# Kernel tuning notes

Measured on AMD Instinct MI355X. Metric: run time of the kernel, lower is better.

## Reference

```python
import jax, jax.numpy as jnp
import numpy as np

NZ, NX, NY = 128, 256, 256
N_GAUSS = 50000
SIGMA_CUTOFF = 3.0
R = 3  # hardcoded stencil radius in voxelize()


def setup_inputs() -> dict:
    key = jax.random.key(0)
    k1, k2, k3, k4 = jax.random.split(key, 4)
    centers = jax.random.uniform(k1, (N_GAUSS, 3), jnp.float32) * 2.0 - 1.0
    log_scales = jnp.full((N_GAUSS, 3), -4.0, jnp.float32)
    rho_real = jax.random.normal(k2, (N_GAUSS,), jnp.float32) * 0.1
    rho_imag = jax.random.normal(k3, (N_GAUSS,), jnp.float32) * 0.1
    # k-space undersampling mask (0/1)
    mask = (jax.random.uniform(k4, (NZ, NX, NY), jnp.float32) < 0.3).astype(jnp.float32)
    return {"mask": mask, "centers": centers, "log_scales": log_scales,
            "rho_real": rho_real, "rho_imag": rho_imag}


def _voxelize(centers, log_scales, rho_real, rho_imag):
    gr = jnp.arange(-R, R + 1)
    kz, kx, ky = jnp.meshgrid(gr, gr, gr, indexing='ij')
    offsets = jnp.stack([kz, kx, ky], axis=-1).reshape(-1, 3)  # [K,3], K=343
    dims = jnp.array([NZ, NX, NY], jnp.int32)
    gsm1 = (dims - 1).astype(jnp.float32)  # grid_size - 1
    # nearest voxel of each gaussian center ([-1,1] -> grid coords)
    ci = jnp.round((centers + 1.0) * 0.5 * gsm1).astype(jnp.int32)  # [M,3]
    ni = ci[:, None, :] + offsets[None, :, :]                        # [M,K,3]
    in_bounds = jnp.all((ni >= 0) & (ni < dims), axis=-1)            # [M,K]
    # neighbor coords back in normalized [-1,1] space
    nc = ni.astype(jnp.float32) / gsm1 * 2.0 - 1.0                   # [M,K,3]
    scales = jnp.exp(log_scales)
    delta = (nc - centers[:, None, :]) / (scales[:, None, :] + 1e-8)
    dist_sq = jnp.sum(delta * delta, axis=-1)                        # [M,K]
    valid = in_bounds & (dist_sq <= SIGMA_CUTOFF ** 2)
    w = jnp.where(valid, jnp.exp(-0.5 * dist_sq), 0.0)               # [M,K]
    vals_r = (rho_real[:, None] * w).ravel()
    vals_i = (rho_imag[:, None] * w).ravel()
    # clip indices for safety; invalid entries contribute 0
    nic = jnp.clip(ni, 0, dims - 1)
    flat = ((nic[..., 0] * NX + nic[..., 1]) * NY + nic[..., 2]).ravel()
    vol_r = jnp.zeros(NZ * NX * NY, jnp.float32).at[flat].add(vals_r).reshape(NZ, NX, NY)
    vol_i = jnp.zeros(NZ * NX * NY, jnp.float32).at[flat].add(vals_i).reshape(NZ, NX, NY)
    return vol_r + 1j * vol_i


def _image_to_kspace(vol):
    # centered orthonormal 3D FFT (standard MRI convention)
    return jnp.fft.fftshift(jnp.fft.fftn(jnp.fft.ifftshift(vol), norm='ortho'))


def reference(mask, centers, log_scales, rho_real, rho_imag):
    volume = _voxelize(centers, log_scales, rho_real, rho_imag)
    kspace_pred = mask * _image_to_kspace(volume)
    return (volume, kspace_pred)
```

## Files before the change

### kernel.cpp

```cpp
#include <hip/hip_runtime.h>
#include <math.h>

#define NZd 128
#define NXd 256
#define NYd 256
#define NVOX (NZd * NXd * NYd)
#define PI_F 3.14159265358979323846f
#define SCALE_ORTHO 3.4526698300124393e-4f
#define CAP 512

__global__ void zero_kernel(float4* __restrict__ p, int n4) {
    int i = blockIdx.x * blockDim.x + threadIdx.x;
    if (i < n4) p[i] = make_float4(0.f, 0.f, 0.f, 0.f);
}
__global__ void zero_ints_kernel(int* __restrict__ p, int n) {
    int i = blockIdx.x * blockDim.x + threadIdx.x;
    if (i < n) p[i] = 0;
}

__global__ void voxelize_kernel(const float* __restrict__ centers,
                                const float* __restrict__ log_scales,
                                const float* __restrict__ rho_r,
                                const float* __restrict__ rho_i,
                                float* __restrict__ vol, int M) {
    long long t = (long long)blockIdx.x * blockDim.x + threadIdx.x;
    if (t >= (long long)M * 343) return;
    int g = (int)(t / 343);
    int k = (int)(t % 343);
    int oz = k / 49 - 3, ox = (k / 7) % 7 - 3, oy = k % 7 - 3;
    float cz = centers[g * 3 + 0], cx = centers[g * 3 + 1], cy = centers[g * 3 + 2];
    int iz = (int)rintf((cz + 1.0f) * 0.5f * 127.0f);
    int ix = (int)rintf((cx + 1.0f) * 0.5f * 255.0f);
    int iy = (int)rintf((cy + 1.0f) * 0.5f * 255.0f);
    int nz = iz + oz, nx = ix + ox, ny = iy + oy;
    if (nz < 0 || nz >= NZd || nx < 0 || nx >= NXd || ny < 0 || ny >= NYd) return;
    float sz = expf(log_scales[g * 3 + 0]) + 1e-8f;
    float sx = expf(log_scales[g * 3 + 1]) + 1e-8f;
    float sy = expf(log_scales[g * 3 + 2]) + 1e-8f;
    float dz = ((float)nz / 127.0f * 2.0f - 1.0f - cz) / sz;
    float dx = ((float)nx / 255.0f * 2.0f - 1.0f - cx) / sx;
    float dy = ((float)ny / 255.0f * 2.0f - 1.0f - cy) / sy;
    float d2 = dz * dz + dx * dx + dy * dy;
    if (d2 > 9.0f) return;
    float w = expf(-0.5f * d2);
    int idx = (nz * NXd + nx) * NYd + ny;
    atomicAdd(&vol[2 * idx + 0], rho_r[g] * w);
    atomicAdd(&vol[2 * idx + 1], rho_i[g] * w);
}

__global__ void copy_real_kernel(const float2* __restrict__ cvol,
                                 float* __restrict__ out) {
    int i = blockIdx.x * blockDim.x + threadIdx.x;
    out[i] = cvol[i].x;
}

__device__ __forceinline__ void center_voxel(const float* __restrict__ centers,
                                             int g, int& iz, int& ix, int& iy) {
    float cz = centers[g * 3 + 0], cx = centers[g * 3 + 1], cy = centers[g * 3 + 2];
    iz = min(max((int)rintf((cz + 1.0f) * 0.5f * 127.0f), 0), 127);
    ix = min(max((int)rintf((cx + 1.0f) * 0.5f * 255.0f), 0), 255);
    iy = min(max((int)rintf((cy + 1.0f) * 0.5f * 255.0f), 0), 255);
}

__global__ void bin_count_kernel(const float* __restrict__ centers,
                                 int* __restrict__ cnt, int M) {
    int g = blockIdx.x * blockDim.x + threadIdx.x;
    if (g >= M) return;
    int iz, ix, iy;
    center_voxel(centers, g, iz, ix, iy);
    atomicAdd(&cnt[((iz >> 4) << 8) | ((ix >> 4) << 4) | (iy >> 4)], 1);
}

__global__ void bin_scan_kernel(const int* __restrict__ cnt,
                                int* __restrict__ off,
                                int* __restrict__ cursor) {
    int lane = threadIdx.x;
    int base = lane << 5;
    int s = 0;
    #pragma unroll
    for (int i = 0; i < 32; i++) s += cnt[base + i];
    int incl = s;
    #pragma unroll
    for (int d = 1; d < 64; d <<= 1) {
        int v = __shfl_up(incl, d, 64);
        if (lane >= d) incl += v;
    }
    int run = incl - s;
    for (int i = 0; i < 32; i++) {
        int c = cnt[base + i];
        off[base + i] = run;
        cursor[base + i] = run;
        run += c;
    }
}

__global__ void bin_scatter_kernel(const float* __restrict__ centers,
                                   const float* __restrict__ log_scales,
                                   const float* __restrict__ rho_r,
                                   const float* __restrict__ rho_i,
                                   int* __restrict__ cursor,
                                   int* __restrict__ ciA,
                                   float* __restrict__ czA, float* __restrict__ cxA,
                                   float* __restrict__ cyA,
                                   float* __restrict__ iszA, float* __restrict__ isxA,
                                   float* __restrict__ isyA,
                                   float* __restrict__ rrA, float* __restrict__ riA,
                                   int M) {
    int g = blockIdx.x * blockDim.x + threadIdx.x;
    if (g >= M) return;
    int iz, ix, iy;
    center_voxel(centers, g, iz, ix, iy);
    int b = ((iz >> 4) << 8) | ((ix >> 4) << 4) | (iy >> 4);
    int pos = atomicAdd(&cursor[b], 1);
    ciA[pos] = (iz << 16) | (ix << 8) | iy;
    czA[pos] = centers[g * 3 + 0];
    cxA[pos] = centers[g * 3 + 1];
    cyA[pos] = centers[g * 3 + 2];
    iszA[pos] = 1.0f / (expf(log_scales[g * 3 + 0]) + 1e-8f);
    isxA[pos] = 1.0f / (expf(log_scales[g * 3 + 1]) + 1e-8f);
    isyA[pos] = 1.0f / (expf(log_scales[g * 3 + 2]) + 1e-8f);
    rrA[pos] = rho_r[g];
    riA[pos] = rho_i[g];
}

__global__ __launch_bounds__(256) void tile_accum_kernel(
        const int* __restrict__ cnt, const int* __restrict__ off,
        const int* __restrict__ ciA,
        const float* __restrict__ czA, const float* __restrict__ cxA,
        const float* __restrict__ cyA,
        const float* __restrict__ iszA, const float* __restrict__ isxA,
        const float* __restrict__ isyA,
        const float* __restrict__ rrA, const float* __restrict__ riA,
        float2* __restrict__ cvol, float* __restrict__ out_vr) {
    __shared__ int   sci[CAP];
    __shared__ float scz[CAP], scx[CAP], scy[CAP];
    __shared__ float sisz[CAP], sisx[CAP], sisy[CAP];
    __shared__ float srr[CAP], sri[CAP];
    __shared__ int wcnt[4];

    int tile = blockIdx.x;
    int ty = tile & 15, tx = (tile >> 4) & 15, tz = tile >> 8;
    int z0 = tz << 3, x0 = tx << 4, y0 = ty << 4;
    int t = threadIdx.x;
    int lane = t & 63, wid = t >> 6;
    int yl = t & 15, xl = t >> 4;
    int nx = x0 + xl, ny = y0 + yl;
    float nxf = (float)nx * (2.0f / 255.0f) - 1.0f;
    float nyf = (float)ny * (2.0f / 255.0f) - 1.0f;

    float accR[8], accI[8], zfs[8];
    #pragma unroll
    for (int i = 0; i < 8; i++) {
        accR[i] = 0.f; accI[i] = 0.f;
        zfs[i] = (float)(z0 + i) * (2.0f / 127.0f) - 1.0f;
    }

    int lc = 0;
    int bzl = max(z0 - 3, 0) >> 4,  bzh = min(z0 + 10, 127) >> 4;
    int bxl = max(x0 - 3, 0) >> 4,  bxh = min(x0 + 18, 255) >> 4;
    int byl = max(y0 - 3, 0) >> 4,  byh = min(y0 + 18, 255) >> 4;

    for (int bz = bzl; bz <= bzh; bz++) {
        for (int bx = bxl; bx <= bxh; bx++) {
            int bl = (bz << 8) | (bx << 4) | byl;
            int bh = (bz << 8) | (bx << 4) | byh;
            int qs = off[bl];
            int qe = off[bh] + cnt[bh];
            for (int q0 = qs; q0 < qe; q0 += 256) {
                int q = q0 + t;
                bool keep = false;
                int cpv = 0;
                float czv, cxv, cyv, iszv, isxv, isyv, rrv, riv;
                if (q < qe) {
                    cpv = ciA[q];
                    int iz = cpv >> 16, ix = (cpv >> 8) & 255, iy = cpv & 255;
                    keep = !(ix + 3 < x0 || ix > x0 + 18 ||
                             iy + 3 < y0 || iy > y0 + 18 ||
                             iz + 3 < z0 || iz > z0 + 10);
                }
                if (keep) {
                    czv = czA[q]; cxv = cxA[q]; cyv = cyA[q];
                    iszv = iszA[q]; isxv = isxA[q]; isyv = isyA[q];
                    rrv = rrA[q]; riv = riA[q];
                }
                unsigned long long m = __ballot(keep);
                __syncthreads();
                if (lane == 0) wcnt[wid] = __popcll(m);
                __syncthreads();
                int ntot = wcnt[0] + wcnt[1] + wcnt[2] + wcnt[3];
                if (lc + ntot > CAP) {
                    for (int u = 0; u < lc; u++) {
                        int cp = sci[u];
                        int iz = cp >> 16, ix = (cp >> 8) & 255, iy = cp & 255;
                        int dxi = nx - ix, dyi = ny - iy;
                        if (dxi < -3 || dxi > 3 || dyi < -3 || dyi > 3) continue;
                        float dxv = (nxf - scx[u]) * sisx[u];
                        float dyv = (nyf - scy[u]) * sisy[u];
                        float dxy2 = dxv * dxv + dyv * dyv;
                        if (dxy2 > 9.0f) continue;
                        float cz_ = scz[u], isz_ = sisz[u];
                        float rr = srr[u], ri = sri[u];
                        int zlo = max(z0, iz - 3) - z0;
                        int zhi = min(z0 + 7, iz + 3) - z0;
                        #pragma unroll
                        for (int zl = 0; zl < 8; zl++) {
                            if (zl >= zlo && zl <= zhi) {
                                float dzv = (zfs[zl] - cz_) * isz_;
                                float d2 = dxy2 + dzv * dzv;
                                if (d2 <= 9.0f) {
                                    float w = __expf(-0.5f * d2);
                                    accR[zl] += rr * w;
                                    accI[zl] += ri * w;
                                }
                            }
                        }
                    }
                    __syncthreads();
                    lc = 0;
                }
                int basew = lc;
                #pragma unroll
                for (int w = 0; w < 4; w++) if (w < wid) basew += wcnt[w];
                if (keep) {
                    int pos = basew + __popcll(m & ((1ULL << lane) - 1));
                    sci[pos] = cpv;
                    scz[pos] = czv; scx[pos] = cxv; scy[pos] = cyv;
                    sisz[pos] = iszv; sisx[pos] = isxv; sisy[pos] = isyv;
                    srr[pos] = rrv; sri[pos] = riv;
                }
                lc += ntot;
            }
        }
    }
    __syncthreads();
    for (int u = 0; u < lc; u++) {
        int cp = sci[u];
        int iz = cp >> 16, ix = (cp >> 8) & 255, iy = cp & 255;
        int dxi = nx - ix, dyi = ny - iy;
        if (dxi < -3 || dxi > 3 || dyi < -3 || dyi > 3) continue;
        float dxv = (nxf - scx[u]) * sisx[u];
        float dyv = (nyf - scy[u]) * sisy[u];
        float dxy2 = dxv * dxv + dyv * dyv;
        if (dxy2 > 9.0f) continue;
        float cz_ = scz[u], isz_ = sisz[u];
        float rr = srr[u], ri = sri[u];
        int zlo = max(z0, iz - 3) - z0;
        int zhi = min(z0 + 7, iz + 3) - z0;
        #pragma unroll
        for (int zl = 0; zl < 8; zl++) {
            if (zl >= zlo && zl <= zhi) {
                float dzv = (zfs[zl] - cz_) * isz_;
                float d2 = dxy2 + dzv * dzv;
                if (d2 <= 9.0f) {
                    float w = __expf(-0.5f * d2);
                    accR[zl] += rr * w;
                    accI[zl] += ri * w;
                }
            }
        }
    }

    #pragma unroll
    for (int zl = 0; zl < 8; zl++) {
        size_t idx = ((size_t)(z0 + zl) * NXd + nx) * NYd + ny;
        cvol[idx] = make_float2(accR[zl], accI[zl]);
        out_vr[idx] = accR[zl];
    }
}

template <int L>
__device__ __forceinline__ void fft_lds(float2* buf) {
    int tid = threadIdx.x;
    for (int half = 1; half < L; half <<= 1) {
        __syncthreads();
        int j = tid & (half - 1);
        int i0 = ((tid ^ j) << 1) | j;
        int i1 = i0 + half;
        float ang = -PI_F * (float)j / (float)half;
        float s, c;
        sincosf(ang, &s, &c);
        float2 a = buf[i0];
        float2 b = buf[i1];
        float tr = c * b.x - s * b.y;
        float ti = c * b.y + s * b.x;
        buf[i0] = make_float2(a.x + tr, a.y + ti);
        buf[i1] = make_float2(a.x - tr, a.y - ti);
    }
    __syncthreads();
}

__global__ void fft_y_kernel(const float2* __restrict__ src,
                             float2* __restrict__ dst) {
    __shared__ float2 buf[256];
    __shared__ float2 tw[128];
    int l = blockIdx.x;
    int tid = threadIdx.x;
    {
        float s, c;
        sincosf(-PI_F * (float)tid / 128.0f, &s, &c);
        tw[tid] = make_float2(c, s);
    }
    int p = ((l >> 8) + l) & 1;
    const float2* s = src + (size_t)l * NYd;
    for (int i = tid; i < 256; i += 128) {
        float2 v = s[i];
        if ((p + i) & 1) { v.x = -v.x; v.y = -v.y; }
        buf[__brev((unsigned)i) >> 24] = v;
    }
    #pragma unroll
    for (int st = 0; st < 8; st++) {
        const int half = 1 << st;
        const int twstep = 128 >> st;
        __syncthreads();
        int j = tid & (half - 1);
        int i0 = ((tid ^ j) << 1) | j;
        int i1 = i0 + half;
        float2 w = tw[j * twstep];
        float2 a = buf[i0];
        float2 b = buf[i1];
        float tr = w.x * b.x - w.y * b.y;
        float ti = w.x * b.y + w.y * b.x;
        buf[i0] = make_float2(a.x + tr, a.y + ti);
        buf[i1] = make_float2(a.x - tr, a.y - ti);
    }
    __syncthreads();
    float2* d = dst + (size_t)l * NYd;
    for (int i = tid; i < 256; i += 128) d[i] = buf[i];
}

__global__ void fft_x_kernel(float2* __restrict__ ks) {
    __shared__ float2 buf[256];
    int l = blockIdx.x;
    int tid = threadIdx.x;
    int z = l >> 8, y = l & 255;
    float2* base = ks + (size_t)z * (NXd * NYd) + y;
    for (int i = tid; i < 256; i += 128)
        buf[__brev((unsigned)i) >> 24] = base[(size_t)i * NYd];
    fft_lds<256>(buf);
    for (int i = tid; i < 256; i += 128)
        base[(size_t)i * NYd] = buf[i];
}
__global__ void fft_z_kernel(float2* __restrict__ ks,
                             const float* __restrict__ mask,
                             float* __restrict__ out_real) {
    __shared__ float2 buf[128];
    int l = blockIdx.x;
    int tid = threadIdx.x;
    float2* base = ks + l;
    for (int i = tid; i < 128; i += 64)
        buf[__brev((unsigned)i) >> 25] = base[(size_t)i * (NXd * NYd)];
    fft_lds<128>(buf);
    int p = ((l >> 8) + l) & 1;
    for (int i = tid; i < 128; i += 64) {
        float2 v = buf[i];
        float sgn = ((p + i) & 1) ? -SCALE_ORTHO : SCALE_ORTHO;
        float m = mask[(size_t)i * (NXd * NYd) + l] * sgn;
        if (out_real) {
            out_real[(size_t)i * (NXd * NYd) + l] = v.x * m;
        } else {
            v.x *= m; v.y *= m;
            base[(size_t)i * (NXd * NYd)] = v;
        }
    }
}

__global__ __launch_bounds__(256) void fft_x16_kernel(float2* __restrict__ ks) {
    __shared__ float2 buf[16][256 + 1];
    __shared__ float2 tw[128];
    int t = threadIdx.x;
    int blk = blockIdx.x;
    int z = blk >> 4;
    int y16 = (blk & 15) << 4;
    if (t < 128) {
        float s, c;
        sincosf(-PI_F * (float)t / 128.0f, &s, &c);
        tw[t] = make_float2(c, s);
    }
    float2* base = ks + (size_t)z * (NXd * NYd) + y16;
    int yl = t & 15, xe0 = t >> 4;
    #pragma unroll
    for (int p = 0; p < 16; p++) {
        int xe = xe0 + (p << 4);
        float2 v = base[(size_t)xe * NYd + yl];
        buf[yl][__brev((unsigned)xe) >> 24] = v;
    }
    int s_ = t & 127;
    int fb0 = t >> 7;
    #pragma unroll
    for (int st = 0; st < 8; st++) {
        const int half = 1 << st;
        const int twstep = 128 >> st;
        __syncthreads();
        int j = s_ & (half - 1);
        int i0 = ((s_ ^ j) << 1) | j;
        int i1 = i0 + half;
        float2 w = tw[j * twstep];
        #pragma unroll
        for (int u = 0; u < 8; u++) {
            int fb = fb0 + (u << 1);
            float2 a = buf[fb][i0];
            float2 b = buf[fb][i1];
            float tr = w.x * b.x - w.y * b.y;
            float ti = w.x * b.y + w.y * b.x;
            buf[fb][i0] = make_float2(a.x + tr, a.y + ti);
            buf[fb][i1] = make_float2(a.x - tr, a.y - ti);
        }
    }
    __syncthreads();
    #pragma unroll
    for (int p = 0; p < 16; p++) {
        int xe = xe0 + (p << 4);
        base[(size_t)xe * NYd + yl] = buf[yl][xe];
    }
}

__global__ __launch_bounds__(256) void fft_z32_kernel(const float2* __restrict__ ks,
                                                      const float* __restrict__ mask,
                                                      float* __restrict__ out_kr) {
    __shared__ float2 buf[32][128 + 1];
    __shared__ float2 tw[64];
    int t = threadIdx.x;
    int blk = blockIdx.x;
    int kx = blk >> 3;
    int ky32 = (blk & 7) << 5;
    if (t < 64) {
        float s, c;
        sincosf(-PI_F * (float)t / 64.0f, &s, &c);
        tw[t] = make_float2(c, s);
    }
    const float2* base = ks + (size_t)kx * NYd + ky32;
    int kyl = t & 31, ze0 = t >> 5;
    #pragma unroll
    for (int p = 0; p < 16; p++) {
        int ze = ze0 + (p << 3);
        float2 v = base[(size_t)ze * (NXd * NYd) + kyl];
        buf[kyl][__brev((unsigned)ze) >> 25] = v;
    }
    int s_ = t & 63;
    int fb0 = t >> 6;
    #pragma unroll
    for (int st = 0; st < 7; st++) {
        const int half = 1 << st;
        const int twstep = 64 >> st;
        __syncthreads();
        int j = s_ & (half - 1);
        int i0 = ((s_ ^ j) << 1) | j;
        int i1 = i0 + half;
        float2 w = tw[j * twstep];
        #pragma unroll
        for (int u = 0; u < 8; u++) {
            int fb = fb0 + (u << 2);
            float2 a = buf[fb][i0];
            float2 b = buf[fb][i1];
            float tr = w.x * b.x - w.y * b.y;
            float ti = w.x * b.y + w.y * b.x;
            buf[fb][i0] = make_float2(a.x + tr, a.y + ti);
            buf[fb][i1] = make_float2(a.x - tr, a.y - ti);
        }
    }
    __syncthreads();
    int ky = ky32 + kyl;
    #pragma unroll
    for (int p = 0; p < 16; p++) {
        int ze = ze0 + (p << 3);
        float2 v = buf[kyl][ze];
        size_t gi = (size_t)ze * (NXd * NYd) + (size_t)kx * NYd + ky;
        float sgn = ((ze + kx + ky) & 1) ? -SCALE_ORTHO : SCALE_ORTHO;
        out_kr[gi] = v.x * (mask[gi] * sgn);
    }
}

extern "C" void kernel_launch(void* const* d_in, const int* in_sizes, int n_in,
                              void* d_out, int out_size, void* d_ws, size_t ws_size,
                              hipStream_t stream) {
    const float* mask       = (const float*)d_in[0];
    const float* centers    = (const float*)d_in[1];
    const float* log_scales = (const float*)d_in[2];
    const float* rho_r      = (const float*)d_in[3];
    const float* rho_i      = (const float*)d_in[4];
    int M = in_sizes[1] / 3;

    bool inter = (out_size >= 4 * NVOX);
    if (!inter) {
        if (out_size < 2 * NVOX || ws_size < (size_t)NVOX * 8) {
            int z4 = out_size / 4;
            if (z4 > 0)
                zero_kernel<<<(z4 + 255) / 256, 256, 0, stream>>>((float4*)d_out, z4);
            return;
        }
        float* out_vr = (float*)d_out;
        float* out_kr = out_vr + NVOX;
        float2* cvol = (float2*)d_ws;

        int Mpad = (M + 63) & ~63;
        bool fast = (8192 + 9LL * Mpad) <= (long long)NVOX;
        if (fast) {
            int* ibase  = (int*)out_kr;
            int* cnt    = ibase;
            int* off    = ibase + 2048;
            int* cursor = ibase + 4096;
            float* fbase = (float*)(ibase + 8192);
            int*   ciA  = (int*)fbase;
            float* czA  = fbase + 1LL * Mpad;
            float* cxA  = fbase + 2LL * Mpad;
            float* cyA  = fbase + 3LL * Mpad;
            float* iszA = fbase + 4LL * Mpad;
            float* isxA = fbase + 5LL * Mpad;
            float* isyA = fbase + 6LL * Mpad;
            float* rrA  = fbase + 7LL * Mpad;
            float* riA  = fbase + 8LL * Mpad;

            zero_ints_kernel<<<8, 256, 0, stream>>>(cnt, 2048);
            bin_count_kernel<<<(M + 255) / 256, 256, 0, stream>>>(centers, cnt, M);
            bin_scan_kernel<<<1, 64, 0, stream>>>(cnt, off, cursor);
            bin_scatter_kernel<<<(M + 255) / 256, 256, 0, stream>>>(
                centers, log_scales, rho_r, rho_i, cursor,
                ciA, czA, cxA, cyA, iszA, isxA, isyA, rrA, riA, M);
            tile_accum_kernel<<<4096, 256, 0, stream>>>(
                cnt, off, ciA, czA, cxA, cyA, iszA, isxA, isyA, rrA, riA,
                cvol, out_vr);
        } else {
            int n4 = (2 * NVOX) / 4;
            zero_kernel<<<(n4 + 255) / 256, 256, 0, stream>>>((float4*)cvol, n4);
            long long total = (long long)M * 343;
            int vb = (int)((total + 255) / 256);
            voxelize_kernel<<<vb, 256, 0, stream>>>(centers, log_scales, rho_r,
                                                    rho_i, (float*)cvol, M);
            copy_real_kernel<<<NVOX / 256, 256, 0, stream>>>(cvol, out_vr);
        }

        fft_y_kernel<<<NZd * NXd, 128, 0, stream>>>(cvol, cvol);
        fft_x16_kernel<<<NZd * 16, 256, 0, stream>>>(cvol);
        fft_z32_kernel<<<NXd * 8, 256, 0, stream>>>(cvol, mask, out_kr);
    } else {
        float2* cvol = (float2*)d_out;
        float2* cks  = cvol + NVOX;
        int n4 = (2 * NVOX) / 4;
        zero_kernel<<<(n4 + 255) / 256, 256, 0, stream>>>((float4*)cvol, n4);
        long long total = (long long)M * 343;
        int vb = (int)((total + 255) / 256);
        voxelize_kernel<<<vb, 256, 0, stream>>>(centers, log_scales, rho_r,
                                                rho_i, (float*)cvol, M);
        fft_y_kernel<<<NZd * NXd, 128, 0, stream>>>(cvol, cks);
        fft_x_kernel<<<NZd * NYd, 128, 0, stream>>>(cks);
        fft_z_kernel<<<NXd * NYd, 64, 0, stream>>>(cks, mask, nullptr);
    }
}
```

Baseline: 201.0 us.

## Scatter gaussians per wavefront into LDS tile accumulators instead of per-voxel gather

The tile accumulation kernel no longer has every thread loop over every candidate gaussian for its own voxel column. Each wavefront now takes one gaussian at a time, with 49 lanes covering its 7x7 xy stencil and looping over z. Contributions go into a shared-memory accumulator tile through LDS float atomics, and the tile is written out at the end. The goal is to drop the wasted per-thread culling of far-away gaussians. In exchange it adds LDS atomic contention and leaves 15 lanes idle per wavefront. The candidate staging capacity shrinks to 192 so the accumulator fits in LDS, which means more flush passes.

```diff
diff --git a/kernel.cpp b/kernel.cpp
--- a/kernel.cpp
+++ b/kernel.cpp
@@ -7,7 +7,7 @@
 #define NVOX (NZd * NXd * NYd)
 #define PI_F 3.14159265358979323846f
 #define SCALE_ORTHO 3.4526698300124393e-4f
-#define CAP 512
+#define CAP 192
 
 __global__ void zero_kernel(float4* __restrict__ p, int n4) {
     int i = blockIdx.x * blockDim.x + threadIdx.x;
@@ -123,6 +123,7 @@
     riA[pos] = rho_i[g];
 }
 
+#define ACCN (8 * 16 * 17)
 __global__ __launch_bounds__(256) void tile_accum_kernel(
         const int* __restrict__ cnt, const int* __restrict__ off,
         const int* __restrict__ ciA,
@@ -132,6 +133,7 @@
         const float* __restrict__ isyA,
         const float* __restrict__ rrA, const float* __restrict__ riA,
         float2* __restrict__ cvol, float* __restrict__ out_vr) {
+    __shared__ float accR[ACCN], accI[ACCN];
     __shared__ int   sci[CAP];
     __shared__ float scz[CAP], scx[CAP], scy[CAP];
     __shared__ float sisz[CAP], sisx[CAP], sisy[CAP];
@@ -143,17 +145,12 @@
     int z0 = tz << 3, x0 = tx << 4, y0 = ty << 4;
     int t = threadIdx.x;
     int lane = t & 63, wid = t >> 6;
-    int yl = t & 15, xl = t >> 4;
-    int nx = x0 + xl, ny = y0 + yl;
-    float nxf = (float)nx * (2.0f / 255.0f) - 1.0f;
-    float nyf = (float)ny * (2.0f / 255.0f) - 1.0f;
-
-    float accR[8], accI[8], zfs[8];
-    #pragma unroll
-    for (int i = 0; i < 8; i++) {
-        accR[i] = 0.f; accI[i] = 0.f;
-        zfs[i] = (float)(z0 + i) * (2.0f / 127.0f) - 1.0f;
-    }
+
+    for (int v = t; v < ACCN; v += 256) { accR[v] = 0.f; accI[v] = 0.f; }
+
+    int dxo = (lane >> 3) - 3;
+    int dyo = (lane & 7) - 3;
+    bool lact = ((lane >> 3) < 7) && ((lane & 7) < 7);
 
     int lc = 0;
     int bzl = max(z0 - 3, 0) >> 4,  bzh = min(z0 + 10, 127) >> 4;
@@ -166,12 +163,12 @@
             int bh = (bz << 8) | (bx << 4) | byh;
             int qs = off[bl];
             int qe = off[bh] + cnt[bh];
-            for (int q0 = qs; q0 < qe; q0 += 256) {
+            for (int q0 = qs; q0 < qe; q0 += CAP) {
                 int q = q0 + t;
                 bool keep = false;
                 int cpv = 0;
                 float czv, cxv, cyv, iszv, isxv, isyv, rrv, riv;
-                if (q < qe) {
+                if (t < CAP && q < qe) {
                     cpv = ciA[q];
                     int iz = cpv >> 16, ix = (cpv >> 8) & 255, iy = cpv & 255;
                     keep = !(ix + 3 < x0 || ix > x0 + 18 ||
@@ -189,29 +186,26 @@
                 __syncthreads();
                 int ntot = wcnt[0] + wcnt[1] + wcnt[2] + wcnt[3];
                 if (lc + ntot > CAP) {
-                    for (int u = 0; u < lc; u++) {
+                    for (int u = wid; u < lc; u += 4) {
                         int cp = sci[u];
                         int iz = cp >> 16, ix = (cp >> 8) & 255, iy = cp & 255;
-                        int dxi = nx - ix, dyi = ny - iy;
-                        if (dxi < -3 || dxi > 3 || dyi < -3 || dyi > 3) continue;
-                        float dxv = (nxf - scx[u]) * sisx[u];
-                        float dyv = (nyf - scy[u]) * sisy[u];
+                        int nx = ix + dxo, ny = iy + dyo;
+                        int xl = nx - x0, yl = ny - y0;
+                        bool ok = lact && (unsigned)xl < 16u && (unsigned)yl < 16u;
+                        float dxv = ((float)nx * (2.0f / 255.0f) - 1.0f - scx[u]) * sisx[u];
+                        float dyv = ((float)ny * (2.0f / 255.0f) - 1.0f - scy[u]) * sisy[u];
                         float dxy2 = dxv * dxv + dyv * dyv;
-                        if (dxy2 > 9.0f) continue;
                         float cz_ = scz[u], isz_ = sisz[u];
                         float rr = srr[u], ri = sri[u];
-                        int zlo = max(z0, iz - 3) - z0;
-                        int zhi = min(z0 + 7, iz + 3) - z0;
-                        #pragma unroll
-                        for (int zl = 0; zl < 8; zl++) {
-                            if (zl >= zlo && zl <= zhi) {
-                                float dzv = (zfs[zl] - cz_) * isz_;
-                                float d2 = dxy2 + dzv * dzv;
-                                if (d2 <= 9.0f) {
-                                    float w = __expf(-0.5f * d2);
-                                    accR[zl] += rr * w;
-                                    accI[zl] += ri * w;
-                                }
+                        int nzlo = max(z0, iz - 3), nzhi = min(z0 + 7, iz + 3);
+                        for (int nz = nzlo; nz <= nzhi; nz++) {
+                            float dzv = ((float)nz * (2.0f / 127.0f) - 1.0f - cz_) * isz_;
+                            float d2 = dxy2 + dzv * dzv;
+                            if (ok && d2 <= 9.0f) {
+                                float w = __expf(-0.5f * d2);
+                                int vi = ((nz - z0) * 16 + xl) * 17 + yl;
+                                atomicAdd(&accR[vi], rr * w);
+                                atomicAdd(&accI[vi], ri * w);
                             }
                         }
                     }
@@ -233,38 +227,38 @@
         }
     }
     __syncthreads();
-    for (int u = 0; u < lc; u++) {
+    for (int u = wid; u < lc; u += 4) {
         int cp = sci[u];
         int iz = cp >> 16, ix = (cp >> 8) & 255, iy = cp & 255;
-        int dxi = nx - ix, dyi = ny - iy;
-        if (dxi < -3 || dxi > 3 || dyi < -3 || dyi > 3) continue;
-        float dxv = (nxf - scx[u]) * sisx[u];
-        float dyv = (nyf - scy[u]) * sisy[u];
+        int nx = ix + dxo, ny = iy + dyo;
+        int xl = nx - x0, yl = ny - y0;
+        bool ok = lact && (unsigned)xl < 16u && (unsigned)yl < 16u;
+        float dxv = ((float)nx * (2.0f / 255.0f) - 1.0f - scx[u]) * sisx[u];
+        float dyv = ((float)ny * (2.0f / 255.0f) - 1.0f - scy[u]) * sisy[u];
         float dxy2 = dxv * dxv + dyv * dyv;
-        if (dxy2 > 9.0f) continue;
         float cz_ = scz[u], isz_ = sisz[u];
         float rr = srr[u], ri = sri[u];
-        int zlo = max(z0, iz - 3) - z0;
-        int zhi = min(z0 + 7, iz + 3) - z0;
-        #pragma unroll
-        for (int zl = 0; zl < 8; zl++) {
-            if (zl >= zlo && zl <= zhi) {
-                float dzv = (zfs[zl] - cz_) * isz_;
-                float d2 = dxy2 + dzv * dzv;
-                if (d2 <= 9.0f) {
-                    float w = __expf(-0.5f * d2);
-                    accR[zl] += rr * w;
-                    accI[zl] += ri * w;
-                }
+        int nzlo = max(z0, iz - 3), nzhi = min(z0 + 7, iz + 3);
+        for (int nz = nzlo; nz <= nzhi; nz++) {
+            float dzv = ((float)nz * (2.0f / 127.0f) - 1.0f - cz_) * isz_;
+            float d2 = dxy2 + dzv * dzv;
+            if (ok && d2 <= 9.0f) {
+                float w = __expf(-0.5f * d2);
+                int vi = ((nz - z0) * 16 + xl) * 17 + yl;
+                atomicAdd(&accR[vi], rr * w);
+                atomicAdd(&accI[vi], ri * w);
             }
         }
     }
-
-    #pragma unroll
-    for (int zl = 0; zl < 8; zl++) {
-        size_t idx = ((size_t)(z0 + zl) * NXd + nx) * NYd + ny;
-        cvol[idx] = make_float2(accR[zl], accI[zl]);
-        out_vr[idx] = accR[zl];
+    __syncthreads();
+
+    for (int v = t; v < 2048; v += 256) {
+        int zl = v >> 8, xl = (v >> 4) & 15, yl = v & 15;
+        int vi = (zl * 16 + xl) * 17 + yl;
+        float r = accR[vi], im = accI[vi];
+        size_t idx = ((size_t)(z0 + zl) * NXd + (x0 + xl)) * NYd + (y0 + yl);
+        cvol[idx] = make_float2(r, im);
+        out_vr[idx] = r;
     }
 }
 
```

After: 323.7 us. +61.1%, slower.
